# Performance work log

Hardware: AMD Instinct MI355X
Metric: run time of the kernel (lower is better)

Reference implementation:

```python
import jax, jax.numpy as jnp
import numpy as np

N_NODES = 100000
N_EDGES = 1600000
D_IN = 128
HID = 128
OUT = 128
N_GRAPHS = 512
BN_EPS = 1e-5


def setup_inputs() -> dict:
    key = jax.random.key(0)
    ks = jax.random.split(key, 24)
    s = 0.05
    inp = {
        "x": jax.random.normal(ks[0], (N_NODES, D_IN), dtype=jnp.float32),
        "edge_index": jax.random.randint(ks[1], (2, N_EDGES), 0, N_NODES, dtype=jnp.int32),
        "batch": jnp.sort(jax.random.randint(ks[2], (N_NODES,), 0, N_GRAPHS, dtype=jnp.int32)),
        # GIN MLP 1
        "W1a": jax.random.normal(ks[3], (D_IN, HID)) * s, "b1a": jnp.zeros((HID,)),
        "W1b": jax.random.normal(ks[4], (HID, HID)) * s, "b1b": jnp.zeros((HID,)),
        "g1": jnp.ones((HID,)), "be1": jnp.zeros((HID,)),
        # GIN MLP 2
        "W2a": jax.random.normal(ks[5], (HID, HID)) * s, "b2a": jnp.zeros((HID,)),
        "W2b": jax.random.normal(ks[6], (HID, HID)) * s, "b2b": jnp.zeros((HID,)),
        "g2": jnp.ones((HID,)), "be2": jnp.zeros((HID,)),
        # GIN MLP 3
        "W3a": jax.random.normal(ks[7], (HID, HID)) * s, "b3a": jnp.zeros((HID,)),
        "W3b": jax.random.normal(ks[8], (HID, HID)) * s, "b3b": jnp.zeros((HID,)),
        "g3": jnp.ones((HID,)), "be3": jnp.zeros((HID,)),
        # final linear
        "Wl": jax.random.normal(ks[9], (3 * HID, OUT)) * s, "bl": jnp.zeros((OUT,)),
    }
    return inp


def _gin(x, edge_index, Wa, ba, Wb, bb):
    # GINConv with eps=0: nn(x_i + sum_{j->i} x_j)
    msgs = x[edge_index[0]]                                  # [E, d] gather
    agg = jax.ops.segment_sum(msgs, edge_index[1], num_segments=N_NODES)
    h = x + agg
    return jax.nn.relu(h @ Wa + ba) @ Wb + bb


def _bn_relu(h, g, b):
    # BatchNorm1d in training mode: biased batch stats over node axis
    m = jnp.mean(h, axis=0)
    v = jnp.mean(jnp.square(h - m), axis=0)
    return jax.nn.relu((h - m) * jax.lax.rsqrt(v + BN_EPS) * g + b)


def _mean_pool(h, batch):
    sums = jax.ops.segment_sum(h, batch, num_segments=N_GRAPHS)       # [G, d]
    cnt = jax.ops.segment_sum(jnp.ones((h.shape[0],), h.dtype), batch,
                              num_segments=N_GRAPHS)
    return sums / jnp.maximum(cnt, 1.0)[:, None]


def reference(x, edge_index, batch,
              W1a, b1a, W1b, b1b, g1, be1,
              W2a, b2a, W2b, b2b, g2, be2,
              W3a, b3a, W3b, b3b, g3, be3,
              Wl, bl):
    h1 = _bn_relu(_gin(x, edge_index, W1a, b1a, W1b, b1b), g1, be1)
    h2 = _bn_relu(_gin(h1, edge_index, W2a, b2a, W2b, b2b), g2, be2)
    h3 = _bn_relu(_gin(h2, edge_index, W3a, b3a, W3b, b3b), g3, be3)
    hf = jnp.concatenate([_mean_pool(h1, batch), _mean_pool(h2, batch),
                          _mean_pool(h3, batch)], axis=1)             # [G, 3H]
    z = hf @ Wl + bl                                                   # [G, O]
    norm = jnp.linalg.norm(z, axis=1, keepdims=True)
    return z / jnp.maximum(norm, 1e-12)
```

## Files before the change

### kernel.cpp

```cpp
#include <hip/hip_runtime.h>
#include <hip/hip_bf16.h>
#include <hip/hip_fp16.h>

#define N_NODES 100000
#define N_EDGES 1600000
#define N_GRAPHS 512
#define BN_EPS 1e-5f
#define NBKT 196
#define PART_CHUNK 4096

typedef float f32x4 __attribute__((ext_vector_type(4)));
typedef _Float16 f16x8 __attribute__((ext_vector_type(8)));


__global__ __launch_bounds__(256) void k_bcnt(const int4* __restrict__ dst4, int* __restrict__ bcnt, int E4) {
    __shared__ int h[NBKT];
    int tid = threadIdx.x;
    for (int i = tid; i < NBKT; i += 256) h[i] = 0;
    __syncthreads();
    for (int t = blockIdx.x * 256 + tid; t < E4; t += gridDim.x * 256) {
        int4 d = dst4[t];
        atomicAdd(&h[d.x >> 9], 1);
        atomicAdd(&h[d.y >> 9], 1);
        atomicAdd(&h[d.z >> 9], 1);
        atomicAdd(&h[d.w >> 9], 1);
    }
    __syncthreads();
    for (int i = tid; i < NBKT; i += 256) {
        int v = h[i];
        if (v) atomicAdd(&bcnt[i], v);
    }
}


__global__ __launch_bounds__(256) void k_bscan(const int* __restrict__ bcnt, int* __restrict__ bbase,
                                               int* __restrict__ gcur) {
    __shared__ int buf[256];
    int tid = threadIdx.x;
    int v = (tid < NBKT) ? bcnt[tid] : 0;
    buf[tid] = v;
    __syncthreads();
    for (int st = 1; st < 256; st <<= 1) {
        int t = (tid >= st) ? buf[tid - st] : 0;
        __syncthreads();
        buf[tid] += t;
        __syncthreads();
    }
    int excl = buf[tid] - v;
    if (tid < NBKT) {
        bbase[tid] = excl;
        gcur[tid] = excl;
    }
    if (tid == NBKT - 1) bbase[NBKT] = excl + v;
}


__global__ __launch_bounds__(256) void k_gstart(const int* __restrict__ batch, int* __restrict__ gcnt, int N) {
    int g = blockIdx.x * 256 + threadIdx.x;
    if (g >= N_GRAPHS) return;
    auto lb = [&](int key) {
        int lo = 0, hi = N;
        while (lo < hi) {
            int mid = (lo + hi) >> 1;
            if (batch[mid] < key) lo = mid + 1; else hi = mid;
        }
        return lo;
    };
    gcnt[g] = lb(g + 1) - lb(g);
}


__global__ __launch_bounds__(256) void k_x2h(const float4* __restrict__ x4, uint4* __restrict__ xh, int n8) {
    int i = blockIdx.x * 256 + threadIdx.x;
    if (i >= n8) return;
    float4 a = x4[2 * i], b = x4[2 * i + 1];
    union { uint4 u4; __half h[8]; } cv;
    cv.h[0] = __float2half(a.x); cv.h[1] = __float2half(a.y);
    cv.h[2] = __float2half(a.z); cv.h[3] = __float2half(a.w);
    cv.h[4] = __float2half(b.x); cv.h[5] = __float2half(b.y);
    cv.h[6] = __float2half(b.z); cv.h[7] = __float2half(b.w);
    xh[i] = cv.u4;
}


__global__ __launch_bounds__(256) void k_part(const int* __restrict__ esrc, const int* __restrict__ edst,
                                              int* __restrict__ gcur, unsigned* __restrict__ ebuf, int E) {
    __shared__ int cnt[256], base[256], scn[256];
    __shared__ unsigned ebufL[PART_CHUNK];
    __shared__ int gposL[PART_CHUNK];
    int tid = threadIdx.x;
    int e0 = blockIdx.x * PART_CHUNK;
    int nv = min(PART_CHUNK, E - e0);
    int src[16], dst[16];
    cnt[tid] = 0;
    __syncthreads();
    const int4* s4 = (const int4*)(esrc + e0);
    const int4* d4 = (const int4*)(edst + e0);
    int n4 = nv >> 2;
#pragma unroll
    for (int t = 0; t < 4; ++t) {
        int i4 = t * 256 + tid;
        if (i4 < n4) {
            int4 s = s4[i4];
            int4 d = d4[i4];
            src[t * 4 + 0] = s.x; src[t * 4 + 1] = s.y; src[t * 4 + 2] = s.z; src[t * 4 + 3] = s.w;
            dst[t * 4 + 0] = d.x; dst[t * 4 + 1] = d.y; dst[t * 4 + 2] = d.z; dst[t * 4 + 3] = d.w;
            atomicAdd(&cnt[d.x >> 9], 1);
            atomicAdd(&cnt[d.y >> 9], 1);
            atomicAdd(&cnt[d.z >> 9], 1);
            atomicAdd(&cnt[d.w >> 9], 1);
        } else {
            dst[t * 4 + 0] = -1; dst[t * 4 + 1] = -1; dst[t * 4 + 2] = -1; dst[t * 4 + 3] = -1;
            src[t * 4 + 0] = 0; src[t * 4 + 1] = 0; src[t * 4 + 2] = 0; src[t * 4 + 3] = 0;
        }
    }
    __syncthreads();
    int c = cnt[tid];
    if (tid < NBKT) base[tid] = atomicAdd(&gcur[tid], c);
    scn[tid] = c;
    __syncthreads();
    for (int st = 1; st < 256; st <<= 1) {
        int t = (tid >= st) ? scn[tid - st] : 0;
        __syncthreads();
        scn[tid] += t;
        __syncthreads();
    }
    scn[tid] -= c;
    __syncthreads();
    cnt[tid] = 0;
    __syncthreads();
#pragma unroll
    for (int t = 0; t < 16; ++t) {
        if (dst[t] >= 0) {
            int b = dst[t] >> 9;
            int r = atomicAdd(&cnt[b], 1);
            int s = scn[b] + r;
            ebufL[s] = (((unsigned)(dst[t] & 511)) << 17) | (unsigned)src[t];
            gposL[s] = base[b] + r;
        }
    }
    __syncthreads();
    for (int s = tid; s < nv; s += 256) ebuf[gposL[s]] = ebufL[s];
}


__global__ __launch_bounds__(256) void k_bucket(const unsigned* __restrict__ ebuf, const int* __restrict__ bbase,
                                                int* __restrict__ off, int* __restrict__ srcs, int N) {
    __shared__ int degL[512];
    __shared__ int s2[256];
    int b = blockIdx.x;
    int n0 = b << 9;
    int nn = min(512, N - n0);
    int tid = threadIdx.x;
    for (int i = tid; i < nn; i += 256) degL[i] = 0;
    __syncthreads();
    int e0 = bbase[b], e1 = bbase[b + 1];
    for (int i = e0 + tid; i < e1; i += 256) atomicAdd(&degL[ebuf[i] >> 17], 1);
    __syncthreads();
    int a0 = (2 * tid < nn) ? degL[2 * tid] : 0;
    int a1 = (2 * tid + 1 < nn) ? degL[2 * tid + 1] : 0;
    int ps = a0 + a1;
    s2[tid] = ps;
    __syncthreads();
    for (int st = 1; st < 256; st <<= 1) {
        int t = (tid >= st) ? s2[tid - st] : 0;
        __syncthreads();
        s2[tid] += t;
        __syncthreads();
    }
    int excl = s2[tid] - ps;
    if (2 * tid < nn) { off[n0 + 2 * tid] = e0 + excl; degL[2 * tid] = e0 + excl; }
    if (2 * tid + 1 < nn) { off[n0 + 2 * tid + 1] = e0 + excl + a0; degL[2 * tid + 1] = e0 + excl + a0; }
    if (b == NBKT - 1 && tid == 0) off[N] = e1;
    __syncthreads();
    for (int i = e0 + tid; i < e1; i += 256) {
        unsigned p = ebuf[i];
        int dl = (int)(p >> 17);
        int pos = atomicAdd(&degL[dl], 1);
        srcs[pos] = (int)(p & 0x1FFFFu);
    }
}


struct W6 { const float* w[6]; };

__global__ __launch_bounds__(256) void k_packw6(W6 ws6, ushort* __restrict__ pk) {
    int m = blockIdx.x >> 6;
    int p = (blockIdx.x & 63) * 256 + threadIdx.x;
    const float* W = ws6.w[m];
    ushort* o = pk + (size_t)m * 16384;
    int j = p & 7, l = (p >> 3) & 63, n = (p >> 9) & 7, kc = p >> 12;
    int row = kc * 32 + ((l >> 4) & 3) * 8 + j;
    int col = n * 16 + (l & 15);
    union { _Float16 h; ushort u; } cv;
    cv.h = (_Float16)W[row * 128 + col];
    o[p] = cv.u;
}


__global__ __launch_bounds__(256) void k_agg(const __half* __restrict__ Xh, float* __restrict__ T,
                                             const int* __restrict__ off, const int* __restrict__ srcs, int N) {
    int gid = blockIdx.x * 256 + threadIdx.x;
    int w = gid >> 6;
    int lane = threadIdx.x & 63;
    int q = lane >> 4;
    int lc = lane & 15;
    int node = w * 4 + q;
    if (node >= N) return;

    const uint4* X16 = (const uint4*)Xh;
    union U { uint4 u4; __half2 h[4]; };

    float2 acc[4];
    {
        U r; r.u4 = X16[(size_t)node * 16 + lc];
#pragma unroll
        for (int k = 0; k < 4; ++k) acc[k] = __half22float2(r.h[k]);
    }

    int s = off[node], e = off[node + 1];
    int j = s;
    for (; j + 7 < e; j += 8) {
        int u0 = srcs[j], u1 = srcs[j + 1], u2 = srcs[j + 2], u3 = srcs[j + 3];
        int u4 = srcs[j + 4], u5 = srcs[j + 5], u6 = srcs[j + 6], u7 = srcs[j + 7];
        U r0, r1, r2, r3, r4, r5, r6, r7;
        r0.u4 = X16[(size_t)u0 * 16 + lc];
        r1.u4 = X16[(size_t)u1 * 16 + lc];
        r2.u4 = X16[(size_t)u2 * 16 + lc];
        r3.u4 = X16[(size_t)u3 * 16 + lc];
        r4.u4 = X16[(size_t)u4 * 16 + lc];
        r5.u4 = X16[(size_t)u5 * 16 + lc];
        r6.u4 = X16[(size_t)u6 * 16 + lc];
        r7.u4 = X16[(size_t)u7 * 16 + lc];
#pragma unroll
        for (int k = 0; k < 4; ++k) {
            float2 f0 = __half22float2(r0.h[k]), f1 = __half22float2(r1.h[k]);
            float2 f2 = __half22float2(r2.h[k]), f3 = __half22float2(r3.h[k]);
            float2 f4 = __half22float2(r4.h[k]), f5 = __half22float2(r5.h[k]);
            float2 f6 = __half22float2(r6.h[k]), f7 = __half22float2(r7.h[k]);
            float2 a01 = make_float2(f0.x + f1.x, f0.y + f1.y);
            float2 a23 = make_float2(f2.x + f3.x, f2.y + f3.y);
            float2 a45 = make_float2(f4.x + f5.x, f4.y + f5.y);
            float2 a67 = make_float2(f6.x + f7.x, f6.y + f7.y);
            acc[k].x += (a01.x + a23.x) + (a45.x + a67.x);
            acc[k].y += (a01.y + a23.y) + (a45.y + a67.y);
        }
    }
    for (; j < e; ++j) {
        U r; r.u4 = X16[(size_t)srcs[j] * 16 + lc];
#pragma unroll
        for (int k = 0; k < 4; ++k) {
            float2 f = __half22float2(r.h[k]);
            acc[k].x += f.x;
            acc[k].y += f.y;
        }
    }

    float4 o0 = make_float4(acc[0].x, acc[0].y, acc[1].x, acc[1].y);
    float4 o1 = make_float4(acc[2].x, acc[2].y, acc[3].x, acc[3].y);
    ((float4*)T)[(size_t)node * 32 + lc * 2] = o0;
    ((float4*)T)[(size_t)node * 32 + lc * 2 + 1] = o1;
}


__global__ __launch_bounds__(256, 4) void k_mlp_pair(const float* __restrict__ A, __half* __restrict__ out,
        const ushort* __restrict__ pk1, const float* __restrict__ b1,
        const ushort* __restrict__ pk2, const float* __restrict__ b2,
        float* __restrict__ stats, int N) {
    __shared__ _Float16 tile[4 * 32 * 128];
    int tid = threadIdx.x;
    int wid = tid >> 6, l = tid & 63;
    int lr = l & 15, lg = l >> 4;
    int r0 = blockIdx.x * 128 + wid * 32;
    int wbase = wid * 32 * 128;

    const f32x4* A4 = (const f32x4*)A;
    const f16x8* B1 = (const f16x8*)pk1;
    const f16x8* B2 = (const f16x8*)pk2;

    f32x4 acc[2][8];
#pragma unroll
    for (int m = 0; m < 2; ++m)
#pragma unroll
        for (int n = 0; n < 8; ++n) acc[m][n] = (f32x4){0.f, 0.f, 0.f, 0.f};

#pragma unroll
    for (int kc = 0; kc < 4; ++kc) {
        f16x8 af[2];
#pragma unroll
        for (int m = 0; m < 2; ++m) {
            int row = min(r0 + m * 16 + lr, N - 1);
            f32x4 v0 = A4[(size_t)row * 32 + kc * 8 + lg * 2];
            f32x4 v1 = A4[(size_t)row * 32 + kc * 8 + lg * 2 + 1];
            af[m][0] = (_Float16)v0.x; af[m][1] = (_Float16)v0.y;
            af[m][2] = (_Float16)v0.z; af[m][3] = (_Float16)v0.w;
            af[m][4] = (_Float16)v1.x; af[m][5] = (_Float16)v1.y;
            af[m][6] = (_Float16)v1.z; af[m][7] = (_Float16)v1.w;
        }
#pragma unroll
        for (int n = 0; n < 8; ++n) {
            f16x8 bf = B1[(kc * 8 + n) * 64 + l];
#pragma unroll
            for (int m = 0; m < 2; ++m)
                acc[m][n] = __builtin_amdgcn_mfma_f32_16x16x32_f16(af[m], bf, acc[m][n], 0, 0, 0);
        }
    }

#pragma unroll
    for (int n = 0; n < 8; ++n) {
        float bv = b1[n * 16 + lr];
        int col = n * 16 + lr;
        int chunk = col >> 3;
        int lo3 = col & 7;
#pragma unroll
        for (int m = 0; m < 2; ++m) {
#pragma unroll
            for (int i = 0; i < 4; ++i) {
                int row = m * 16 + lg * 4 + i;
                float v = fmaxf(acc[m][n][i] + bv, 0.f);
                tile[wbase + row * 128 + ((chunk ^ (row & 15)) << 3) + lo3] = (_Float16)v;
            }
        }
    }
    __syncthreads();

#pragma unroll
    for (int m = 0; m < 2; ++m)
#pragma unroll
        for (int n = 0; n < 8; ++n) acc[m][n] = (f32x4){0.f, 0.f, 0.f, 0.f};

#pragma unroll
    for (int kc = 0; kc < 4; ++kc) {
        f16x8 af[2];
#pragma unroll
        for (int m = 0; m < 2; ++m) {
            int row = m * 16 + lr;
            af[m] = *(const f16x8*)&tile[wbase + row * 128 + (((kc * 4 + lg) ^ (row & 15)) << 3)];
        }
#pragma unroll
        for (int n = 0; n < 8; ++n) {
            f16x8 bf = B2[(kc * 8 + n) * 64 + l];
#pragma unroll
            for (int m = 0; m < 2; ++m)
                acc[m][n] = __builtin_amdgcn_mfma_f32_16x16x32_f16(af[m], bf, acc[m][n], 0, 0, 0);
        }
    }
    __syncthreads();

    float s1[8], s2[8];
#pragma unroll
    for (int n = 0; n < 8; ++n) { s1[n] = 0.f; s2[n] = 0.f; }

#pragma unroll
    for (int n = 0; n < 8; ++n) {
        float bv = b2[n * 16 + lr];
#pragma unroll
        for (int m = 0; m < 2; ++m) {
#pragma unroll
            for (int i = 0; i < 4; ++i) {
                int r = r0 + m * 16 + lg * 4 + i;
                if (r < N) {
                    float v = acc[m][n][i] + bv;
                    s1[n] += v;
                    s2[n] += v * v;
                    out[(size_t)r * 128 + n * 16 + lr] = __float2half(v);
                }
            }
        }
    }

    float* ls = (float*)tile;
#pragma unroll
    for (int n = 0; n < 8; ++n) {
        float a = s1[n], b = s2[n];
        a += __shfl_xor(a, 16, 64); a += __shfl_xor(a, 32, 64);
        b += __shfl_xor(b, 16, 64); b += __shfl_xor(b, 32, 64);
        if (lg == 0) {
            ls[wid * 256 + n * 16 + lr] = a;
            ls[wid * 256 + 128 + n * 16 + lr] = b;
        }
    }
    __syncthreads();
    float t = ls[tid] + ls[256 + tid] + ls[512 + tid] + ls[768 + tid];
    atomicAdd(&stats[tid], t);
}


__global__ __launch_bounds__(128) void k_bnpool(const __half* __restrict__ h, __half* __restrict__ hp,
                                                const float* __restrict__ stats,
                                                const float* __restrict__ gamma, const float* __restrict__ beta,
                                                const int* __restrict__ batch, float* __restrict__ pool,
                                                int loff, int N) {
    int c = threadIdx.x;
    const float invN = 1.0f / (float)N;
    float mean = stats[c] * invN;
    float var = stats[128 + c] * invN - mean * mean;
    float rstd = rsqrtf(var + BN_EPS);
    float gsc = gamma[c] * rstd;
    float bs = beta[c] - mean * gsc;

    int r0 = blockIdx.x * 64;
    int r1 = min(r0 + 64, N);
    float acc = 0.f;
    int curg = -1;
    for (int r = r0; r < r1; ++r) {
        float v = __half2float(h[(size_t)r * 128 + c]);
        float hv = fmaxf(fmaf(v, gsc, bs), 0.f);
        hp[(size_t)r * 128 + c] = __float2half(hv);
        int g = batch[r];
        if (g != curg) {
            if (curg >= 0) atomicAdd(&pool[(size_t)curg * 384 + loff + c], acc);
            curg = g;
            acc = hv;
        } else {
            acc += hv;
        }
    }
    if (curg >= 0) atomicAdd(&pool[(size_t)curg * 384 + loff + c], acc);
}


__global__ __launch_bounds__(128) void k_final(const float* __restrict__ pool, const int* __restrict__ gcnt,
                                               const float* __restrict__ Wl, const float* __restrict__ bl,
                                               float* __restrict__ out) {
    __shared__ float sh[384];
    __shared__ float red[128];
    int g = blockIdx.x;
    int tid = threadIdx.x;
    float inv = 1.0f / fmaxf((float)gcnt[g], 1.0f);
    for (int t = tid; t < 384; t += 128) sh[t] = pool[(size_t)g * 384 + t] * inv;
    __syncthreads();
    float acc = bl[tid];
    for (int k = 0; k < 384; ++k) acc = fmaf(sh[k], Wl[(size_t)k * 128 + tid], acc);
    red[tid] = acc * acc;
    __syncthreads();
    for (int s = 64; s > 0; s >>= 1) {
        if (tid < s) red[tid] += red[tid + s];
        __syncthreads();
    }
    float norm = sqrtf(red[0]);
    float scale = 1.0f / fmaxf(norm, 1e-12f);
    out[(size_t)g * 128 + tid] = acc * scale;
}


extern "C" void kernel_launch(void* const* d_in, const int* in_sizes, int n_in,
                              void* d_out, int out_size, void* d_ws, size_t ws_size,
                              hipStream_t stream) {
    const float* x = (const float*)d_in[0];
    const int* edge_index = (const int*)d_in[1];
    const int* batch = (const int*)d_in[2];
    const float* Wa[3] = {(const float*)d_in[3], (const float*)d_in[9], (const float*)d_in[15]};
    const float* ba[3] = {(const float*)d_in[4], (const float*)d_in[10], (const float*)d_in[16]};
    const float* Wb[3] = {(const float*)d_in[5], (const float*)d_in[11], (const float*)d_in[17]};
    const float* bb[3] = {(const float*)d_in[6], (const float*)d_in[12], (const float*)d_in[18]};
    const float* gm[3] = {(const float*)d_in[7], (const float*)d_in[13], (const float*)d_in[19]};
    const float* be[3] = {(const float*)d_in[8], (const float*)d_in[14], (const float*)d_in[20]};
    const float* Wl = (const float*)d_in[21];
    const float* bl = (const float*)d_in[22];
    float* out = (float*)d_out;

    const int N = N_NODES, E = N_EDGES, G = N_GRAPHS;
    const int* e_src = edge_index;
    const int* e_dst = edge_index + E;

    char* ws = (char*)d_ws;
    size_t o = 0;
    auto alloc = [&](size_t bytes) -> char* {
        char* p = ws + o;
        o = (o + bytes + 255) & ~(size_t)255;
        return p;
    };
    int* off = (int*)alloc((size_t)(N + 1) * 4);
    int* srcs = (int*)alloc((size_t)E * 4);
    int* gcnt = (int*)alloc((size_t)G * 4);
    int* bcnt = (int*)alloc(256 * 4);
    int* bbase = (int*)alloc(256 * 4);
    int* gcur = (int*)alloc(256 * 4);
    float* stats = (float*)alloc(3 * 256 * 4);
    ushort* wpk = (ushort*)alloc(6 * 16384 * 2);
    float* pool = (float*)alloc((size_t)G * 384 * 4);
    float* T = (float*)alloc((size_t)N * 128 * 4);
    __half* B0 = (__half*)alloc((size_t)N * 128 * 2);
    __half* B1 = (__half*)alloc((size_t)N * 128 * 2);
    unsigned* ebuf = (unsigned*)T;
    (void)ws_size;

    hipMemsetAsync(bcnt, 0, 256 * 4, stream);
    hipMemsetAsync(stats, 0, 3 * 256 * 4, stream);
    hipMemsetAsync(pool, 0, (size_t)G * 384 * 4, stream);

    const int E4 = E / 4;

    k_bcnt<<<256, 256, 0, stream>>>((const int4*)e_dst, bcnt, E4);
    k_bscan<<<1, 256, 0, stream>>>(bcnt, bbase, gcur);
    k_gstart<<<2, 256, 0, stream>>>(batch, gcnt, N);
    k_part<<<(E + PART_CHUNK - 1) / PART_CHUNK, 256, 0, stream>>>(e_src, e_dst, gcur, ebuf, E);
    k_bucket<<<NBKT, 256, 0, stream>>>(ebuf, bbase, off, srcs, N);

    const int n8 = N * 128 / 8;
    k_x2h<<<(n8 + 255) / 256, 256, 0, stream>>>((const float4*)x, (uint4*)B0, n8);

    W6 w6;
    w6.w[0] = Wa[0]; w6.w[1] = Wb[0]; w6.w[2] = Wa[1];
    w6.w[3] = Wb[1]; w6.w[4] = Wa[2]; w6.w[5] = Wb[2];
    k_packw6<<<384, 256, 0, stream>>>(w6, wpk);

    const int aggBlocks = ((N + 3) / 4 * 64 + 255) / 256;
    const int mlpBlocks = (N + 127) / 128;
    const int bnBlocks = (N + 63) / 64;

    for (int l = 0; l < 3; ++l) {
        float* statsl = stats + l * 256;
        k_agg<<<aggBlocks, 256, 0, stream>>>(B0, T, off, srcs, N);
        k_mlp_pair<<<mlpBlocks, 256, 0, stream>>>(T, B1, wpk + (size_t)(2 * l) * 16384, ba[l],
                                                  wpk + (size_t)(2 * l + 1) * 16384, bb[l], statsl, N);
        k_bnpool<<<bnBlocks, 128, 0, stream>>>(B1, B0, statsl, gm[l], be[l], batch, pool, l * 128, N);
    }

    k_final<<<G, 128, 0, stream>>>(pool, gcnt, Wl, bl, out);
}
```

Before: 503.0 us.

## Fuse neighbor aggregation into GIN MLP kernel via shared-memory fp16 tile

Merges the gather-sum aggregation kernel into the MLP kernel. Each wave aggregates its 32 rows straight into the swizzled LDS tile as fp16, and the first GEMM reads its A operand from that tile, so the fp32 intermediate T no longer goes through global memory. It also removes a __syncthreads, which looks safe because each wave only touches its own tile region. The bnpool kernel now runs 256 threads per block, each half covering 32 rows. The trade-off is that the irregular gather now sits inside a register-heavy MFMA kernel, which may reduce latency hiding, and the aggregate is rounded to fp16 before the GEMM.

New measurement: 454.4 us. -9.7%, faster.

```diff
diff --git a/kernel.cpp b/kernel.cpp
--- a/kernel.cpp
+++ b/kernel.cpp
@@ -198,72 +198,8 @@
 }
 
 
-__global__ __launch_bounds__(256) void k_agg(const __half* __restrict__ Xh, float* __restrict__ T,
-                                             const int* __restrict__ off, const int* __restrict__ srcs, int N) {
-    int gid = blockIdx.x * 256 + threadIdx.x;
-    int w = gid >> 6;
-    int lane = threadIdx.x & 63;
-    int q = lane >> 4;
-    int lc = lane & 15;
-    int node = w * 4 + q;
-    if (node >= N) return;
-
-    const uint4* X16 = (const uint4*)Xh;
-    union U { uint4 u4; __half2 h[4]; };
-
-    float2 acc[4];
-    {
-        U r; r.u4 = X16[(size_t)node * 16 + lc];
-#pragma unroll
-        for (int k = 0; k < 4; ++k) acc[k] = __half22float2(r.h[k]);
-    }
-
-    int s = off[node], e = off[node + 1];
-    int j = s;
-    for (; j + 7 < e; j += 8) {
-        int u0 = srcs[j], u1 = srcs[j + 1], u2 = srcs[j + 2], u3 = srcs[j + 3];
-        int u4 = srcs[j + 4], u5 = srcs[j + 5], u6 = srcs[j + 6], u7 = srcs[j + 7];
-        U r0, r1, r2, r3, r4, r5, r6, r7;
-        r0.u4 = X16[(size_t)u0 * 16 + lc];
-        r1.u4 = X16[(size_t)u1 * 16 + lc];
-        r2.u4 = X16[(size_t)u2 * 16 + lc];
-        r3.u4 = X16[(size_t)u3 * 16 + lc];
-        r4.u4 = X16[(size_t)u4 * 16 + lc];
-        r5.u4 = X16[(size_t)u5 * 16 + lc];
-        r6.u4 = X16[(size_t)u6 * 16 + lc];
-        r7.u4 = X16[(size_t)u7 * 16 + lc];
-#pragma unroll
-        for (int k = 0; k < 4; ++k) {
-            float2 f0 = __half22float2(r0.h[k]), f1 = __half22float2(r1.h[k]);
-            float2 f2 = __half22float2(r2.h[k]), f3 = __half22float2(r3.h[k]);
-            float2 f4 = __half22float2(r4.h[k]), f5 = __half22float2(r5.h[k]);
-            float2 f6 = __half22float2(r6.h[k]), f7 = __half22float2(r7.h[k]);
-            float2 a01 = make_float2(f0.x + f1.x, f0.y + f1.y);
-            float2 a23 = make_float2(f2.x + f3.x, f2.y + f3.y);
-            float2 a45 = make_float2(f4.x + f5.x, f4.y + f5.y);
-            float2 a67 = make_float2(f6.x + f7.x, f6.y + f7.y);
-            acc[k].x += (a01.x + a23.x) + (a45.x + a67.x);
-            acc[k].y += (a01.y + a23.y) + (a45.y + a67.y);
-        }
-    }
-    for (; j < e; ++j) {
-        U r; r.u4 = X16[(size_t)srcs[j] * 16 + lc];
-#pragma unroll
-        for (int k = 0; k < 4; ++k) {
-            float2 f = __half22float2(r.h[k]);
-            acc[k].x += f.x;
-            acc[k].y += f.y;
-        }
-    }
-
-    float4 o0 = make_float4(acc[0].x, acc[0].y, acc[1].x, acc[1].y);
-    float4 o1 = make_float4(acc[2].x, acc[2].y, acc[3].x, acc[3].y);
-    ((float4*)T)[(size_t)node * 32 + lc * 2] = o0;
-    ((float4*)T)[(size_t)node * 32 + lc * 2 + 1] = o1;
-}
-
-
-__global__ __launch_bounds__(256, 4) void k_mlp_pair(const float* __restrict__ A, __half* __restrict__ out,
+__global__ __launch_bounds__(256, 4) void k_gin(const __half* __restrict__ Xh, __half* __restrict__ out,
+        const int* __restrict__ off, const int* __restrict__ srcs,
         const ushort* __restrict__ pk1, const float* __restrict__ b1,
         const ushort* __restrict__ pk2, const float* __restrict__ b2,
         float* __restrict__ stats, int N) {
@@ -274,7 +210,63 @@
     int r0 = blockIdx.x * 128 + wid * 32;
     int wbase = wid * 32 * 128;
 
-    const f32x4* A4 = (const f32x4*)A;
+    const uint4* X16 = (const uint4*)Xh;
+    union U { uint4 u4; __half2 h[4]; };
+
+    for (int g = 0; g < 8; ++g) {
+        int row = g * 4 + lg;
+        int node = r0 + row;
+        float2 acc[4];
+        if (node < N) {
+            U r; r.u4 = X16[(size_t)node * 16 + lr];
+#pragma unroll
+            for (int k = 0; k < 4; ++k) acc[k] = __half22float2(r.h[k]);
+            int s = off[node], e = off[node + 1];
+            int j = s;
+            for (; j + 7 < e; j += 8) {
+                int u0 = srcs[j], u1 = srcs[j + 1], u2 = srcs[j + 2], u3 = srcs[j + 3];
+                int u4 = srcs[j + 4], u5 = srcs[j + 5], u6 = srcs[j + 6], u7 = srcs[j + 7];
+                U r0_, r1_, r2_, r3_, r4_, r5_, r6_, r7_;
+                r0_.u4 = X16[(size_t)u0 * 16 + lr];
+                r1_.u4 = X16[(size_t)u1 * 16 + lr];
+                r2_.u4 = X16[(size_t)u2 * 16 + lr];
+                r3_.u4 = X16[(size_t)u3 * 16 + lr];
+                r4_.u4 = X16[(size_t)u4 * 16 + lr];
+                r5_.u4 = X16[(size_t)u5 * 16 + lr];
+                r6_.u4 = X16[(size_t)u6 * 16 + lr];
+                r7_.u4 = X16[(size_t)u7 * 16 + lr];
+#pragma unroll
+                for (int k = 0; k < 4; ++k) {
+                    float2 f0 = __half22float2(r0_.h[k]), f1 = __half22float2(r1_.h[k]);
+                    float2 f2 = __half22float2(r2_.h[k]), f3 = __half22float2(r3_.h[k]);
+                    float2 f4 = __half22float2(r4_.h[k]), f5 = __half22float2(r5_.h[k]);
+                    float2 f6 = __half22float2(r6_.h[k]), f7 = __half22float2(r7_.h[k]);
+                    acc[k].x += ((f0.x + f1.x) + (f2.x + f3.x)) + ((f4.x + f5.x) + (f6.x + f7.x));
+                    acc[k].y += ((f0.y + f1.y) + (f2.y + f3.y)) + ((f4.y + f5.y) + (f6.y + f7.y));
+                }
+            }
+            for (; j < e; ++j) {
+                U r2; r2.u4 = X16[(size_t)srcs[j] * 16 + lr];
+#pragma unroll
+                for (int k = 0; k < 4; ++k) {
+                    float2 f = __half22float2(r2.h[k]);
+                    acc[k].x += f.x;
+                    acc[k].y += f.y;
+                }
+            }
+        } else {
+#pragma unroll
+            for (int k = 0; k < 4; ++k) acc[k] = make_float2(0.f, 0.f);
+        }
+        f16x8 v;
+#pragma unroll
+        for (int k = 0; k < 4; ++k) {
+            v[2 * k] = (_Float16)acc[k].x;
+            v[2 * k + 1] = (_Float16)acc[k].y;
+        }
+        *(f16x8*)&tile[wbase + row * 128 + ((lr ^ (row & 15)) << 3)] = v;
+    }
+
     const f16x8* B1 = (const f16x8*)pk1;
     const f16x8* B2 = (const f16x8*)pk2;
 
@@ -289,13 +281,8 @@
         f16x8 af[2];
 #pragma unroll
         for (int m = 0; m < 2; ++m) {
-            int row = min(r0 + m * 16 + lr, N - 1);
-            f32x4 v0 = A4[(size_t)row * 32 + kc * 8 + lg * 2];
-            f32x4 v1 = A4[(size_t)row * 32 + kc * 8 + lg * 2 + 1];
-            af[m][0] = (_Float16)v0.x; af[m][1] = (_Float16)v0.y;
-            af[m][2] = (_Float16)v0.z; af[m][3] = (_Float16)v0.w;
-            af[m][4] = (_Float16)v1.x; af[m][5] = (_Float16)v1.y;
-            af[m][6] = (_Float16)v1.z; af[m][7] = (_Float16)v1.w;
+            int row = m * 16 + lr;
+            af[m] = *(const f16x8*)&tile[wbase + row * 128 + (((kc * 4 + lg) ^ (row & 15)) << 3)];
         }
 #pragma unroll
         for (int n = 0; n < 8; ++n) {
@@ -322,7 +309,6 @@
             }
         }
     }
-    __syncthreads();
 
 #pragma unroll
     for (int m = 0; m < 2; ++m)
@@ -386,12 +372,13 @@
 }
 
 
-__global__ __launch_bounds__(128) void k_bnpool(const __half* __restrict__ h, __half* __restrict__ hp,
+__global__ __launch_bounds__(256) void k_bnpool(const __half* __restrict__ h, __half* __restrict__ hp,
                                                 const float* __restrict__ stats,
                                                 const float* __restrict__ gamma, const float* __restrict__ beta,
                                                 const int* __restrict__ batch, float* __restrict__ pool,
                                                 int loff, int N) {
-    int c = threadIdx.x;
+    int c = threadIdx.x & 127;
+    int half = threadIdx.x >> 7;
     const float invN = 1.0f / (float)N;
     float mean = stats[c] * invN;
     float var = stats[128 + c] * invN - mean * mean;
@@ -399,8 +386,8 @@
     float gsc = gamma[c] * rstd;
     float bs = beta[c] - mean * gsc;
 
-    int r0 = blockIdx.x * 64;
-    int r1 = min(r0 + 64, N);
+    int r0 = blockIdx.x * 64 + half * 32;
+    int r1 = min(r0 + 32, N);
     float acc = 0.f;
     int curg = -1;
     for (int r = r0; r < r1; ++r) {
@@ -480,10 +467,9 @@
     float* stats = (float*)alloc(3 * 256 * 4);
     ushort* wpk = (ushort*)alloc(6 * 16384 * 2);
     float* pool = (float*)alloc((size_t)G * 384 * 4);
-    float* T = (float*)alloc((size_t)N * 128 * 4);
     __half* B0 = (__half*)alloc((size_t)N * 128 * 2);
     __half* B1 = (__half*)alloc((size_t)N * 128 * 2);
-    unsigned* ebuf = (unsigned*)T;
+    unsigned* ebuf = (unsigned*)B1;
     (void)ws_size;
 
     hipMemsetAsync(bcnt, 0, 256 * 4, stream);
@@ -506,16 +492,15 @@
     w6.w[3] = Wb[1]; w6.w[4] = Wa[2]; w6.w[5] = Wb[2];
     k_packw6<<<384, 256, 0, stream>>>(w6, wpk);
 
-    const int aggBlocks = ((N + 3) / 4 * 64 + 255) / 256;
-    const int mlpBlocks = (N + 127) / 128;
+    const int ginBlocks = (N + 127) / 128;
     const int bnBlocks = (N + 63) / 64;
 
     for (int l = 0; l < 3; ++l) {
         float* statsl = stats + l * 256;
-        k_agg<<<aggBlocks, 256, 0, stream>>>(B0, T, off, srcs, N);
-        k_mlp_pair<<<mlpBlocks, 256, 0, stream>>>(T, B1, wpk + (size_t)(2 * l) * 16384, ba[l],
-                                                  wpk + (size_t)(2 * l + 1) * 16384, bb[l], statsl, N);
-        k_bnpool<<<bnBlocks, 128, 0, stream>>>(B1, B0, statsl, gm[l], be[l], batch, pool, l * 128, N);
+        k_gin<<<ginBlocks, 256, 0, stream>>>(B0, B1, off, srcs,
+                                             wpk + (size_t)(2 * l) * 16384, ba[l],
+                                             wpk + (size_t)(2 * l + 1) * 16384, bb[l], statsl, N);
+        k_bnpool<<<bnBlocks, 256, 0, stream>>>(B1, B0, statsl, gm[l], be[l], batch, pool, l * 128, N);
     }
 
     k_final<<<G, 128, 0, stream>>>(pool, gcnt, Wl, bl, out);
```

## Store aggregation output in fp16 and stage MLP input through LDS

Applied to the files above, without the earlier changes.

The neighbour-sum buffer is now written as fp16 rather than fp32, which halves the bytes written by the aggregation kernel and read back by the MLP kernel at each of the three layers. The MLP kernel loads its fp16 input rows with coalesced vector loads into a swizzled per-wave LDS tile and reads its MFMA operands from there. A block barrier is dropped because each wave only touches its own tile region. The BN/pool kernel now runs 256 threads per block, each half covering 32 rows, for more parallelism at the cost of more pool atomics. Rounding the aggregated sums to fp16 adds precision loss before the first matmul.

New measurement: 481.9 us. 1.04x faster.

```diff
diff --git a/kernel.cpp b/kernel.cpp
--- a/kernel.cpp
+++ b/kernel.cpp
@@ -198,7 +198,7 @@
 }
 
 
-__global__ __launch_bounds__(256) void k_agg(const __half* __restrict__ Xh, float* __restrict__ T,
+__global__ __launch_bounds__(256) void k_agg(const __half* __restrict__ Xh, __half* __restrict__ T,
                                              const int* __restrict__ off, const int* __restrict__ srcs, int N) {
     int gid = blockIdx.x * 256 + threadIdx.x;
     int w = gid >> 6;
@@ -238,12 +238,8 @@
             float2 f2 = __half22float2(r2.h[k]), f3 = __half22float2(r3.h[k]);
             float2 f4 = __half22float2(r4.h[k]), f5 = __half22float2(r5.h[k]);
             float2 f6 = __half22float2(r6.h[k]), f7 = __half22float2(r7.h[k]);
-            float2 a01 = make_float2(f0.x + f1.x, f0.y + f1.y);
-            float2 a23 = make_float2(f2.x + f3.x, f2.y + f3.y);
-            float2 a45 = make_float2(f4.x + f5.x, f4.y + f5.y);
-            float2 a67 = make_float2(f6.x + f7.x, f6.y + f7.y);
-            acc[k].x += (a01.x + a23.x) + (a45.x + a67.x);
-            acc[k].y += (a01.y + a23.y) + (a45.y + a67.y);
+            acc[k].x += ((f0.x + f1.x) + (f2.x + f3.x)) + ((f4.x + f5.x) + (f6.x + f7.x));
+            acc[k].y += ((f0.y + f1.y) + (f2.y + f3.y)) + ((f4.y + f5.y) + (f6.y + f7.y));
         }
     }
     for (; j < e; ++j) {
@@ -256,14 +252,17 @@
         }
     }
 
-    float4 o0 = make_float4(acc[0].x, acc[0].y, acc[1].x, acc[1].y);
-    float4 o1 = make_float4(acc[2].x, acc[2].y, acc[3].x, acc[3].y);
-    ((float4*)T)[(size_t)node * 32 + lc * 2] = o0;
-    ((float4*)T)[(size_t)node * 32 + lc * 2 + 1] = o1;
-}
-
-
-__global__ __launch_bounds__(256, 4) void k_mlp_pair(const float* __restrict__ A, __half* __restrict__ out,
+    f16x8 v;
+#pragma unroll
+    for (int k = 0; k < 4; ++k) {
+        v[2 * k] = (_Float16)acc[k].x;
+        v[2 * k + 1] = (_Float16)acc[k].y;
+    }
+    *(f16x8*)&((_Float16*)T)[(size_t)node * 128 + lc * 8] = v;
+}
+
+
+__global__ __launch_bounds__(256, 4) void k_mlp(const __half* __restrict__ T, __half* __restrict__ out,
         const ushort* __restrict__ pk1, const float* __restrict__ b1,
         const ushort* __restrict__ pk2, const float* __restrict__ b2,
         float* __restrict__ stats, int N) {
@@ -274,7 +273,18 @@
     int r0 = blockIdx.x * 128 + wid * 32;
     int wbase = wid * 32 * 128;
 
-    const f32x4* A4 = (const f32x4*)A;
+    const f16x8* T8 = (const f16x8*)T;
+
+#pragma unroll
+    for (int i = 0; i < 8; ++i) {
+        int idx = i * 64 + l;
+        int row = idx >> 4;
+        int chunk = idx & 15;
+        int grow = min(r0 + row, N - 1);
+        f16x8 v = T8[(size_t)grow * 16 + chunk];
+        *(f16x8*)&tile[wbase + row * 128 + ((chunk ^ (row & 15)) << 3)] = v;
+    }
+
     const f16x8* B1 = (const f16x8*)pk1;
     const f16x8* B2 = (const f16x8*)pk2;
 
@@ -289,13 +299,8 @@
         f16x8 af[2];
 #pragma unroll
         for (int m = 0; m < 2; ++m) {
-            int row = min(r0 + m * 16 + lr, N - 1);
-            f32x4 v0 = A4[(size_t)row * 32 + kc * 8 + lg * 2];
-            f32x4 v1 = A4[(size_t)row * 32 + kc * 8 + lg * 2 + 1];
-            af[m][0] = (_Float16)v0.x; af[m][1] = (_Float16)v0.y;
-            af[m][2] = (_Float16)v0.z; af[m][3] = (_Float16)v0.w;
-            af[m][4] = (_Float16)v1.x; af[m][5] = (_Float16)v1.y;
-            af[m][6] = (_Float16)v1.z; af[m][7] = (_Float16)v1.w;
+            int row = m * 16 + lr;
+            af[m] = *(const f16x8*)&tile[wbase + row * 128 + (((kc * 4 + lg) ^ (row & 15)) << 3)];
         }
 #pragma unroll
         for (int n = 0; n < 8; ++n) {
@@ -322,7 +327,6 @@
             }
         }
     }
-    __syncthreads();
 
 #pragma unroll
     for (int m = 0; m < 2; ++m)
@@ -386,12 +390,13 @@
 }
 
 
-__global__ __launch_bounds__(128) void k_bnpool(const __half* __restrict__ h, __half* __restrict__ hp,
+__global__ __launch_bounds__(256) void k_bnpool(const __half* __restrict__ h, __half* __restrict__ hp,
                                                 const float* __restrict__ stats,
                                                 const float* __restrict__ gamma, const float* __restrict__ beta,
                                                 const int* __restrict__ batch, float* __restrict__ pool,
                                                 int loff, int N) {
-    int c = threadIdx.x;
+    int c = threadIdx.x & 127;
+    int half = threadIdx.x >> 7;
     const float invN = 1.0f / (float)N;
     float mean = stats[c] * invN;
     float var = stats[128 + c] * invN - mean * mean;
@@ -399,8 +404,8 @@
     float gsc = gamma[c] * rstd;
     float bs = beta[c] - mean * gsc;
 
-    int r0 = blockIdx.x * 64;
-    int r1 = min(r0 + 64, N);
+    int r0 = blockIdx.x * 64 + half * 32;
+    int r1 = min(r0 + 32, N);
     float acc = 0.f;
     int curg = -1;
     for (int r = r0; r < r1; ++r) {
@@ -480,10 +485,10 @@
     float* stats = (float*)alloc(3 * 256 * 4);
     ushort* wpk = (ushort*)alloc(6 * 16384 * 2);
     float* pool = (float*)alloc((size_t)G * 384 * 4);
-    float* T = (float*)alloc((size_t)N * 128 * 4);
     __half* B0 = (__half*)alloc((size_t)N * 128 * 2);
     __half* B1 = (__half*)alloc((size_t)N * 128 * 2);
-    unsigned* ebuf = (unsigned*)T;
+    __half* T16 = (__half*)alloc((size_t)N * 128 * 2);
+    unsigned* ebuf = (unsigned*)T16;
     (void)ws_size;
 
     hipMemsetAsync(bcnt, 0, 256 * 4, stream);
@@ -512,10 +517,10 @@
 
     for (int l = 0; l < 3; ++l) {
         float* statsl = stats + l * 256;
-        k_agg<<<aggBlocks, 256, 0, stream>>>(B0, T, off, srcs, N);
-        k_mlp_pair<<<mlpBlocks, 256, 0, stream>>>(T, B1, wpk + (size_t)(2 * l) * 16384, ba[l],
-                                                  wpk + (size_t)(2 * l + 1) * 16384, bb[l], statsl, N);
-        k_bnpool<<<bnBlocks, 128, 0, stream>>>(B1, B0, statsl, gm[l], be[l], batch, pool, l * 128, N);
+        k_agg<<<aggBlocks, 256, 0, stream>>>(B0, T16, off, srcs, N);
+        k_mlp<<<mlpBlocks, 256, 0, stream>>>(T16, B1, wpk + (size_t)(2 * l) * 16384, ba[l],
+                                             wpk + (size_t)(2 * l + 1) * 16384, bb[l], statsl, N);
+        k_bnpool<<<bnBlocks, 256, 0, stream>>>(B1, B0, statsl, gm[l], be[l], batch, pool, l * 128, N);
     }
 
     k_final<<<G, 128, 0, stream>>>(pool, gcnt, Wl, bl, out);
```
